# Optimization experiments

Measured on AMD Instinct MI355X. Metric: run time of the kernel, lower is better.

The kernel has to match this reference:

```python
import jax, jax.numpy as jnp
import numpy as np

N0, N1, N2 = 10000, 40000, 160000
E1, E2 = 240000, 960000
C_IN, C_MID, C_OUT = 64, 32, 16  # up_convs = [64, 32, 16]


def _basis(pseudo):
    """Open quadratic B-spline basis, kernel_size=3, degree=2, dim=2.
    With kernel_size-degree == 1, v = pseudo in [0,1) and all 3 basis fns per dim
    are active with fixed indices 0..2, so the 2-D product gives 9 weights/edge."""
    t = pseudo  # [E, 2]
    b = jnp.stack([0.5 * (1.0 - t) ** 2, -t * t + t + 0.5, 0.5 * t * t], axis=-1)  # [E,2,3]
    return (b[:, 0, :, None] * b[:, 1, None, :]).reshape(t.shape[0], 9)  # [E, 9]


def _spline_conv(x, src, dst, basis, W, R, b, n):
    # x: [N, Cin], W: [9, Cin, Cout], R: [Cin, Cout], b: [Cout]
    xs = x[src]  # [E, Cin] gather
    m = basis[:, 0:1] * (xs @ W[0])
    for k in range(1, 9):  # fixed small kernel loop; avoids [E,9,Cout] blowup
        m = m + basis[:, k:k + 1] * (xs @ W[k])
    agg = jax.ops.segment_sum(m, dst, num_segments=n)  # aggr='add'
    return agg + x @ R + b


def _up_level(x_coarse, unpool, edge, pseudo, skip, W1, R1, b1, W2, R2, b2):
    n = unpool.shape[0]
    x = x_coarse[unpool]          # MeshUnpool: copy coarse features to fine verts
    basis = _basis(pseudo)
    src, dst = edge[0], edge[1]
    h = jax.nn.relu(_spline_conv(x, src, dst, basis, W1, R1, b1, n))
    h = jnp.concatenate([h, skip], axis=1)  # [n, 2*Cout] == Cin
    h = jax.nn.relu(_spline_conv(h, src, dst, basis, W1, R1, b1, n))  # conv1 reused
    h = jax.nn.relu(_spline_conv(h, src, dst, basis, W2, R2, b2, n))
    return h


def setup_inputs() -> dict:
    key = jax.random.key(0)
    ks = jax.random.split(key, 24)
    s = 0.05
    inp = {
        'x0': jax.random.normal(ks[0], (N0, C_IN), jnp.float32),
        'unpool1': jax.random.randint(ks[1], (N1,), 0, N0),
        'edge1': jax.random.randint(ks[2], (2, E1), 0, N1),
        'pseudo1': jax.random.uniform(ks[3], (E1, 2), jnp.float32),
        'skip1': jax.random.normal(ks[4], (N1, C_MID), jnp.float32),
        'unpool2': jax.random.randint(ks[5], (N2,), 0, N1),
        'edge2': jax.random.randint(ks[6], (2, E2), 0, N2),
        'pseudo2': jax.random.uniform(ks[7], (E2, 2), jnp.float32),
        'skip2': jax.random.normal(ks[8], (N2, C_OUT), jnp.float32),
        # level 1 (UpConv 64 -> 32)
        'W1a': jax.random.normal(ks[9], (9, C_IN, C_MID), jnp.float32) * s,
        'R1a': jax.random.normal(ks[10], (C_IN, C_MID), jnp.float32) * s,
        'b1a': jax.random.normal(ks[11], (C_MID,), jnp.float32) * s,
        'W2a': jax.random.normal(ks[12], (9, C_MID, C_MID), jnp.float32) * s,
        'R2a': jax.random.normal(ks[13], (C_MID, C_MID), jnp.float32) * s,
        'b2a': jax.random.normal(ks[14], (C_MID,), jnp.float32) * s,
        # level 2 (UpConv 32 -> 16)
        'W1b': jax.random.normal(ks[15], (9, C_MID, C_OUT), jnp.float32) * s,
        'R1b': jax.random.normal(ks[16], (C_MID, C_OUT), jnp.float32) * s,
        'b1b': jax.random.normal(ks[17], (C_OUT,), jnp.float32) * s,
        'W2b': jax.random.normal(ks[18], (9, C_OUT, C_OUT), jnp.float32) * s,
        'R2b': jax.random.normal(ks[19], (C_OUT, C_OUT), jnp.float32) * s,
        'b2b': jax.random.normal(ks[20], (C_OUT,), jnp.float32) * s,
    }
    return inp


def reference(x0, unpool1, edge1, pseudo1, skip1, unpool2, edge2, pseudo2, skip2,
              W1a, R1a, b1a, W2a, R2a, b2a, W1b, R1b, b1b, W2b, R2b, b2b):
    h1 = _up_level(x0, unpool1, edge1, pseudo1, skip1, W1a, R1a, b1a, W2a, R2a, b2a)
    h2 = _up_level(h1, unpool2, edge2, pseudo2, skip2, W1b, R1b, b1b, W2b, R2b, b2b)
    return h2
```

## Files before the change

kernel.cpp:

```cpp
#include <hip/hip_runtime.h>
#include <stdint.h>

typedef __bf16 bf16x8 __attribute__((ext_vector_type(8)));
typedef __bf16 bf16x4 __attribute__((ext_vector_type(4)));
typedef float  f32x4  __attribute__((ext_vector_type(4)));

__global__ void k_up_f2b(const float4* __restrict__ xin, const int* __restrict__ up,
                         __bf16* __restrict__ xout, int N, int rowF4, int rowC) {
  int i = blockIdx.x * 256 + threadIdx.x;
  if (i >= N * rowF4) return;
  int n = i / rowF4, j = i - n * rowF4;
  float4 v = xin[(size_t)up[n] * rowF4 + j];
  bf16x4 o = {(__bf16)v.x, (__bf16)v.y, (__bf16)v.z, (__bf16)v.w};
  *reinterpret_cast<bf16x4*>(xout + (size_t)n * rowC + j * 4) = o;
}

__global__ void k_up_b2b(const uint4* __restrict__ xin, const int* __restrict__ up,
                         uint4* __restrict__ xout, int N, int rowU4) {
  int i = blockIdx.x * 256 + threadIdx.x;
  if (i >= N * rowU4) return;
  int n = i / rowU4, j = i - n * rowU4;
  xout[i] = xin[(size_t)up[n] * rowU4 + j];
}

__global__ __launch_bounds__(256) void k_bhist(const int* __restrict__ dst, int E,
                                               int* __restrict__ bcnt, int nbk) {
  __shared__ int h[256];
  int t = threadIdx.x;
  h[t] = 0;
  __syncthreads();
  int e0 = blockIdx.x * 2048 + t * 8;
  if (e0 + 8 <= E) {
    int4 a = *reinterpret_cast<const int4*>(dst + e0);
    int4 b = *reinterpret_cast<const int4*>(dst + e0 + 4);
    atomicAdd(&h[a.x >> 10], 1); atomicAdd(&h[a.y >> 10], 1);
    atomicAdd(&h[a.z >> 10], 1); atomicAdd(&h[a.w >> 10], 1);
    atomicAdd(&h[b.x >> 10], 1); atomicAdd(&h[b.y >> 10], 1);
    atomicAdd(&h[b.z >> 10], 1); atomicAdd(&h[b.w >> 10], 1);
  } else {
    for (int j = 0; j < 8; ++j)
      if (e0 + j < E) atomicAdd(&h[dst[e0 + j] >> 10], 1);
  }
  __syncthreads();
  if (t < nbk && h[t]) atomicAdd(&bcnt[t], h[t]);
}

__global__ void k_bscan(const int* __restrict__ bcnt, int nbk, int E,
                        int* __restrict__ bstart, int* __restrict__ bcur) {
  __shared__ int wsum[4];
  int t = threadIdx.x, lane = t & 63, w = t >> 6;
  int v = (t < nbk) ? bcnt[t] : 0;
  int x = v;
  #pragma unroll
  for (int o = 1; o < 64; o <<= 1) { int y = __shfl_up(x, o, 64); if (lane >= o) x += y; }
  if (lane == 63) wsum[w] = x;
  __syncthreads();
  int wpre = 0;
  #pragma unroll
  for (int k = 0; k < 4; ++k) if (k < w) wpre += wsum[k];
  int excl = wpre + x - v;
  if (t < nbk) { bstart[t] = excl; bcur[t] = excl; }
  if (t == 0) bstart[nbk] = E;
}

__global__ __launch_bounds__(256) void k_bpart(const int* __restrict__ src,
                        const int* __restrict__ dst, const float2* __restrict__ pse,
                        int E, int* __restrict__ bcur, uint2* __restrict__ ebuf, int nbk) {
  __shared__ int h[256];
  __shared__ int base[256];
  int t = threadIdx.x;
  h[t] = 0;
  __syncthreads();
  int e0 = blockIdx.x * 2048 + t * 8;
  int d[8], rank[8];
  bool full = (e0 + 8 <= E);
  if (full) {
    int4 a = *reinterpret_cast<const int4*>(dst + e0);
    int4 b = *reinterpret_cast<const int4*>(dst + e0 + 4);
    d[0] = a.x; d[1] = a.y; d[2] = a.z; d[3] = a.w;
    d[4] = b.x; d[5] = b.y; d[6] = b.z; d[7] = b.w;
    #pragma unroll
    for (int j = 0; j < 8; ++j) rank[j] = atomicAdd(&h[d[j] >> 10], 1);
  } else {
    #pragma unroll
    for (int j = 0; j < 8; ++j)
      if (e0 + j < E) { d[j] = dst[e0 + j]; rank[j] = atomicAdd(&h[d[j] >> 10], 1); }
  }
  __syncthreads();
  if (t < nbk && h[t]) base[t] = atomicAdd(&bcur[t], h[t]);
  __syncthreads();
  if (full) {
    int4 a = *reinterpret_cast<const int4*>(src + e0);
    int4 b = *reinterpret_cast<const int4*>(src + e0 + 4);
    int s[8] = {a.x, a.y, a.z, a.w, b.x, b.y, b.z, b.w};
    float2 p[8];
    #pragma unroll
    for (int j = 0; j < 8; ++j) p[j] = pse[e0 + j];
    #pragma unroll
    for (int j = 0; j < 8; ++j) {
      int bkt = d[j] >> 10, dloc = d[j] & 1023;
      union { uint u; _Float16 hh[2]; } cv;
      cv.hh[0] = (_Float16)p[j].x; cv.hh[1] = (_Float16)p[j].y;
      ebuf[base[bkt] + rank[j]] = make_uint2((uint)s[j] | ((uint)dloc << 18), cv.u);
    }
  } else {
    #pragma unroll
    for (int j = 0; j < 8; ++j) {
      if (e0 + j >= E) continue;
      int bkt = d[j] >> 10, dloc = d[j] & 1023;
      float2 p = pse[e0 + j];
      union { uint u; _Float16 hh[2]; } cv;
      cv.hh[0] = (_Float16)p.x; cv.hh[1] = (_Float16)p.y;
      ebuf[base[bkt] + rank[j]] = make_uint2((uint)src[e0 + j] | ((uint)dloc << 18), cv.u);
    }
  }
}

__global__ __launch_bounds__(256) void k_bcsr(const int* __restrict__ bstart,
                        const uint2* __restrict__ ebuf, uint2* __restrict__ epk,
                        int* __restrict__ off, int N, int E, int nbk) {
  __shared__ int cnt[1024];
  __shared__ int excl[1024];
  __shared__ int cur[1024];
  __shared__ int wsum[4];
  int b = blockIdx.x, t = threadIdx.x;
  int e0 = bstart[b], e1 = bstart[b + 1];
  #pragma unroll
  for (int k = 0; k < 4; ++k) { cnt[t * 4 + k] = 0; cur[t * 4 + k] = 0; }
  __syncthreads();
  for (int i = e0 + t; i < e1; i += 256)
    atomicAdd(&cnt[(ebuf[i].x >> 18) & 1023], 1);
  __syncthreads();
  int lane = t & 63, w = t >> 6;
  int i0 = t * 4;
  int c0 = cnt[i0], c1 = cnt[i0 + 1], c2 = cnt[i0 + 2], c3 = cnt[i0 + 3];
  int s = c0 + c1 + c2 + c3, x = s;
  #pragma unroll
  for (int o = 1; o < 64; o <<= 1) { int y = __shfl_up(x, o, 64); if (lane >= o) x += y; }
  if (lane == 63) wsum[w] = x;
  __syncthreads();
  int wpre = 0;
  #pragma unroll
  for (int k = 0; k < 4; ++k) if (k < w) wpre += wsum[k];
  int ex = wpre + x - s;
  excl[i0] = ex; excl[i0 + 1] = ex + c0; excl[i0 + 2] = ex + c0 + c1; excl[i0 + 3] = ex + c0 + c1 + c2;
  int dg0 = b * 1024;
  int exv[4] = {ex, ex + c0, ex + c0 + c1, ex + c0 + c1 + c2};
  #pragma unroll
  for (int k = 0; k < 4; ++k) {
    int d = dg0 + i0 + k;
    if (d < N) off[d] = e0 + exv[k];
  }
  __syncthreads();
  for (int i = e0 + t; i < e1; i += 256) {
    uint2 r = ebuf[i];
    int dloc = (r.x >> 18) & 1023;
    int rk = atomicAdd(&cur[dloc], 1);
    epk[e0 + excl[dloc] + rk] = make_uint2(r.x & 0x3FFFFu, r.y);
  }
  if (b == nbk - 1 && t == 0) off[N] = E;
}

__global__ void k_packall(const float* __restrict__ W1a, const float* __restrict__ R1a,
                          const float* __restrict__ W2a, const float* __restrict__ R2a,
                          const float* __restrict__ W1b, const float* __restrict__ R1b,
                          const float* __restrict__ W2b, const float* __restrict__ R2b,
                          __bf16* __restrict__ BpA, __bf16* __restrict__ BpB,
                          __bf16* __restrict__ BpC, __bf16* __restrict__ BpD) {
  int o = blockIdx.x * 256 + threadIdx.x;
  const float *W, *R; __bf16* Bp; int Cin, Cout;
  if (o < 20480)      { W = W1a; R = R1a; Bp = BpA; Cin = 64; Cout = 32; }
  else if (o < 30720) { W = W2a; R = R2a; Bp = BpB; Cin = 32; Cout = 32; o -= 20480; }
  else if (o < 35840) { W = W1b; R = R1b; Bp = BpC; Cin = 32; Cout = 16; o -= 30720; }
  else if (o < 38400) { W = W2b; R = R2b; Bp = BpD; Cin = 16; Cout = 16; o -= 35840; }
  else return;
  int CT = Cout / 16;
  int j = o & 7, lane = (o >> 3) & 63, tile = o >> 9;
  int ct = tile % CT, kc = tile / CT;
  int k = kc * 32 + ((lane >> 4) * 8) + j;
  int n = ct * 16 + (lane & 15);
  float v;
  if (k < 9 * Cin) { int k9 = k / Cin, cin = k - k9 * Cin; v = W[(k9 * Cin + cin) * Cout + n]; }
  else             { v = R[(k - 9 * Cin) * Cout + n]; }
  Bp[o] = (__bf16)v;
}

template<int Cin, int Cout, bool OUTF32, bool HAS_SKIP>
__global__ __launch_bounds__(256, 6) void k_conv(const int* __restrict__ off,
                        const uint2* __restrict__ epk,
                        const __bf16* __restrict__ X, const __bf16* __restrict__ Bp,
                        const float* __restrict__ bias, const float* __restrict__ skip,
                        void* __restrict__ outv, int N, int outStride) {
  constexpr int LPD = Cin / 4;
  constexpr int DPB = 256 / LPD;
  constexpr int K   = 10 * Cin;
  constexpr int KP2 = K + 8;
  constexpr int NT  = DPB / 16;
  constexpr int KC  = K / 32;
  constexpr int CT  = Cout / 16;
  constexpr int UNITS = NT * CT;

  __shared__ __bf16 As[DPB * KP2];

  int t = threadIdx.x;
  int g = t / LPD, sub = t % LPD;
  int d = blockIdx.x * DPB + g;

  float acc[9][4];
  #pragma unroll
  for (int k = 0; k < 9; ++k)
    #pragma unroll
    for (int v = 0; v < 4; ++v) acc[k][v] = 0.f;
  bf16x4 xd = {};

  if (d < N) {
    xd = *reinterpret_cast<const bf16x4*>(X + (size_t)d * Cin + sub * 4);
    int b0 = off[d], b1 = off[d + 1];
    int i = b0;
    for (; i + 4 <= b1; i += 4) {
      uint2 e0 = epk[i], e1 = epk[i + 1], e2 = epk[i + 2], e3 = epk[i + 3];
      bf16x4 xf0 = *reinterpret_cast<const bf16x4*>(X + (size_t)e0.x * Cin + sub * 4);
      bf16x4 xf1 = *reinterpret_cast<const bf16x4*>(X + (size_t)e1.x * Cin + sub * 4);
      bf16x4 xf2 = *reinterpret_cast<const bf16x4*>(X + (size_t)e2.x * Cin + sub * 4);
      bf16x4 xf3 = *reinterpret_cast<const bf16x4*>(X + (size_t)e3.x * Cin + sub * 4);
      uint ps[4] = {e0.y, e1.y, e2.y, e3.y};
      bf16x4 xfs[4] = {xf0, xf1, xf2, xf3};
      #pragma unroll
      for (int c = 0; c < 4; ++c) {
        union { uint u; _Float16 h[2]; } cv; cv.u = ps[c];
        float t0 = (float)cv.h[0], t1 = (float)cv.h[1];
        float u0 = 1.f - t0;
        float wi[3] = {0.5f * u0 * u0, -t0 * t0 + t0 + 0.5f, 0.5f * t0 * t0};
        float u1 = 1.f - t1;
        float wj[3] = {0.5f * u1 * u1, -t1 * t1 + t1 + 0.5f, 0.5f * t1 * t1};
        float xfv[4];
        #pragma unroll
        for (int v = 0; v < 4; ++v) xfv[v] = (float)xfs[c][v];
        #pragma unroll
        for (int ki = 0; ki < 3; ++ki)
          #pragma unroll
          for (int kj = 0; kj < 3; ++kj) {
            float w = wi[ki] * wj[kj];
            #pragma unroll
            for (int v = 0; v < 4; ++v)
              acc[ki * 3 + kj][v] += w * xfv[v];
          }
      }
    }
    for (; i < b1; ++i) {
      uint2 ep = epk[i];
      bf16x4 xf = *reinterpret_cast<const bf16x4*>(X + (size_t)ep.x * Cin + sub * 4);
      union { uint u; _Float16 h[2]; } cv; cv.u = ep.y;
      float t0 = (float)cv.h[0], t1 = (float)cv.h[1];
      float u0 = 1.f - t0;
      float wi[3] = {0.5f * u0 * u0, -t0 * t0 + t0 + 0.5f, 0.5f * t0 * t0};
      float u1 = 1.f - t1;
      float wj[3] = {0.5f * u1 * u1, -t1 * t1 + t1 + 0.5f, 0.5f * t1 * t1};
      float xfv[4];
      #pragma unroll
      for (int v = 0; v < 4; ++v) xfv[v] = (float)xf[v];
      #pragma unroll
      for (int ki = 0; ki < 3; ++ki)
        #pragma unroll
        for (int kj = 0; kj < 3; ++kj) {
          float w = wi[ki] * wj[kj];
          #pragma unroll
          for (int v = 0; v < 4; ++v)
            acc[ki * 3 + kj][v] += w * xfv[v];
        }
    }
  }

  __bf16* row = As + (size_t)g * KP2;
  #pragma unroll
  for (int k = 0; k < 9; ++k) {
    bf16x4 tmp;
    #pragma unroll
    for (int v = 0; v < 4; ++v) tmp[v] = (__bf16)acc[k][v];
    *reinterpret_cast<bf16x4*>(row + k * Cin + sub * 4) = tmp;
  }
  *reinterpret_cast<bf16x4*>(row + 9 * Cin + sub * 4) = xd;
  __syncthreads();

  int lane = t & 63, wave = t >> 6;
  int c15 = lane & 15, q = lane >> 4;
  for (int u = wave; u < UNITS; u += 4) {
    int tile = u / CT, ct = u - tile * CT;
    const __bf16* arow = As + (size_t)(tile * 16 + c15) * KP2 + q * 8;
    f32x4 a4 = {0.f, 0.f, 0.f, 0.f};
    #pragma unroll
    for (int kc = 0; kc < KC; ++kc) {
      bf16x8 a = *reinterpret_cast<const bf16x8*>(arow + kc * 32);
      bf16x8 b = *reinterpret_cast<const bf16x8*>(Bp + ((size_t)(kc * CT + ct) * 64 + lane) * 8);
      a4 = __builtin_amdgcn_mfma_f32_16x16x32_bf16(a, b, a4, 0, 0, 0);
    }
    int cout = ct * 16 + c15;
    float bb = bias[cout];
    #pragma unroll
    for (int r = 0; r < 4; ++r) {
      int m = q * 4 + r;
      int dd = blockIdx.x * DPB + tile * 16 + m;
      if (dd < N) {
        float vv = fmaxf(a4[r] + bb, 0.f);
        if constexpr (OUTF32)
          ((float*)outv)[(size_t)dd * outStride + cout] = vv;
        else
          ((__bf16*)outv)[(size_t)dd * outStride + cout] = (__bf16)vv;
        if constexpr (HAS_SKIP) {
          float sv = skip[(size_t)dd * Cout + cout];
          ((__bf16*)outv)[(size_t)dd * outStride + Cout + cout] = (__bf16)sv;
        }
      }
    }
  }
}

extern "C" void kernel_launch(void* const* d_in, const int* in_sizes, int n_in,
                              void* d_out, int out_size, void* d_ws, size_t ws_size,
                              hipStream_t stream) {
  const float* x0      = (const float*)d_in[0];
  const int*   up1     = (const int*)d_in[1];
  const int*   edge1   = (const int*)d_in[2];
  const float* pseudo1 = (const float*)d_in[3];
  const float* skip1   = (const float*)d_in[4];
  const int*   up2     = (const int*)d_in[5];
  const int*   edge2   = (const int*)d_in[6];
  const float* pseudo2 = (const float*)d_in[7];
  const float* skip2   = (const float*)d_in[8];
  const float* W1a = (const float*)d_in[9];
  const float* R1a = (const float*)d_in[10];
  const float* b1a = (const float*)d_in[11];
  const float* W2a = (const float*)d_in[12];
  const float* R2a = (const float*)d_in[13];
  const float* b2a = (const float*)d_in[14];
  const float* W1b = (const float*)d_in[15];
  const float* R1b = (const float*)d_in[16];
  const float* b1b = (const float*)d_in[17];
  const float* W2b = (const float*)d_in[18];
  const float* R2b = (const float*)d_in[19];
  const float* b2b = (const float*)d_in[20];

  const int N1 = 40000, N2 = 160000, E1 = 240000, E2 = 960000;
  const int NBK1 = (N1 + 1023) / 1024;
  const int NBK2 = (N2 + 1023) / 1024;

  char* ws = (char*)d_ws;
  __bf16* x1    = (__bf16*)(ws);
  __bf16* xcat1 = (__bf16*)(ws +  5120000);
  __bf16* x3    = (__bf16*)(ws + 10240000);
  __bf16* h1    = (__bf16*)(ws + 12800000);
  __bf16* x2    = (__bf16*)(ws + 15360000);
  __bf16* xcat2 = (__bf16*)(ws + 25600000);
  __bf16* x6    = (__bf16*)(ws + 35840000);
  int* off    = (int*)(ws + 40960000);
  uint2* ebuf = (uint2*)(ws + 41600016);
  uint2* epk  = (uint2*)(ws + 49280016);
  int* bcnt   = (int*)(ws + 56960016);
  int* bstart = (int*)(ws + 56961040);
  int* bcur   = (int*)(ws + 56962080);
  __bf16* BpA = (__bf16*)(ws + 56963104);
  __bf16* BpB = (__bf16*)(ws + 57004064);
  __bf16* BpC = (__bf16*)(ws + 57024544);
  __bf16* BpD = (__bf16*)(ws + 57034784);

  k_packall<<<150, 256, 0, stream>>>(W1a, R1a, W2a, R2a, W1b, R1b, W2b, R2b,
                                     BpA, BpB, BpC, BpD);

  k_up_f2b<<<N1 * 16 / 256, 256, 0, stream>>>((const float4*)x0, up1, x1, N1, 16, 64);

  hipMemsetAsync(bcnt, 0, 256 * 4, stream);
  k_bhist<<<(E1 + 2047) / 2048, 256, 0, stream>>>(edge1 + E1, E1, bcnt, NBK1);
  k_bscan<<<1, 256, 0, stream>>>(bcnt, NBK1, E1, bstart, bcur);
  k_bpart<<<(E1 + 2047) / 2048, 256, 0, stream>>>(edge1, edge1 + E1, (const float2*)pseudo1,
                                                  E1, bcur, ebuf, NBK1);
  k_bcsr<<<NBK1, 256, 0, stream>>>(bstart, ebuf, epk, off, N1, E1, NBK1);

  k_conv<64, 32, false, true><<<N1 / 16, 256, 0, stream>>>(off, epk, x1, BpA, b1a, skip1, xcat1, N1, 64);
  k_conv<64, 32, false, false><<<N1 / 16, 256, 0, stream>>>(off, epk, xcat1, BpA, b1a, nullptr, x3, N1, 32);
  k_conv<32, 32, false, false><<<N1 / 32, 256, 0, stream>>>(off, epk, x3, BpB, b2a, nullptr, h1, N1, 32);

  k_up_b2b<<<N2 * 4 / 256, 256, 0, stream>>>((const uint4*)h1, up2, (uint4*)x2, N2, 4);

  hipMemsetAsync(bcnt, 0, 256 * 4, stream);
  k_bhist<<<(E2 + 2047) / 2048, 256, 0, stream>>>(edge2 + E2, E2, bcnt, NBK2);
  k_bscan<<<1, 256, 0, stream>>>(bcnt, NBK2, E2, bstart, bcur);
  k_bpart<<<(E2 + 2047) / 2048, 256, 0, stream>>>(edge2, edge2 + E2, (const float2*)pseudo2,
                                                  E2, bcur, ebuf, NBK2);
  k_bcsr<<<NBK2, 256, 0, stream>>>(bstart, ebuf, epk, off, N2, E2, NBK2);

  k_conv<32, 16, false, true><<<N2 / 32, 256, 0, stream>>>(off, epk, x2, BpC, b1b, skip2, xcat2, N2, 32);
  k_conv<32, 16, false, false><<<N2 / 32, 256, 0, stream>>>(off, epk, xcat2, BpC, b1b, nullptr, x6, N2, 16);
  k_conv<16, 16, true, false><<<N2 / 64, 256, 0, stream>>>(off, epk, x6, BpD, b2b, nullptr, d_out, N2, 16);
}
```

Baseline: 357.2 us.

## Merge preprocessing for both levels into combined multi-role kernels

```diff
diff --git a/kernel.cpp b/kernel.cpp
--- a/kernel.cpp
+++ b/kernel.cpp
@@ -4,16 +4,6 @@
 typedef __bf16 bf16x8 __attribute__((ext_vector_type(8)));
 typedef __bf16 bf16x4 __attribute__((ext_vector_type(4)));
 typedef float  f32x4  __attribute__((ext_vector_type(4)));
-
-__global__ void k_up_f2b(const float4* __restrict__ xin, const int* __restrict__ up,
-                         __bf16* __restrict__ xout, int N, int rowF4, int rowC) {
-  int i = blockIdx.x * 256 + threadIdx.x;
-  if (i >= N * rowF4) return;
-  int n = i / rowF4, j = i - n * rowF4;
-  float4 v = xin[(size_t)up[n] * rowF4 + j];
-  bf16x4 o = {(__bf16)v.x, (__bf16)v.y, (__bf16)v.z, (__bf16)v.w};
-  *reinterpret_cast<bf16x4*>(xout + (size_t)n * rowC + j * 4) = o;
-}
 
 __global__ void k_up_b2b(const uint4* __restrict__ xin, const int* __restrict__ up,
                          uint4* __restrict__ xout, int N, int rowU4) {
@@ -23,151 +13,10 @@
   xout[i] = xin[(size_t)up[n] * rowU4 + j];
 }
 
-__global__ __launch_bounds__(256) void k_bhist(const int* __restrict__ dst, int E,
-                                               int* __restrict__ bcnt, int nbk) {
-  __shared__ int h[256];
-  int t = threadIdx.x;
-  h[t] = 0;
-  __syncthreads();
-  int e0 = blockIdx.x * 2048 + t * 8;
-  if (e0 + 8 <= E) {
-    int4 a = *reinterpret_cast<const int4*>(dst + e0);
-    int4 b = *reinterpret_cast<const int4*>(dst + e0 + 4);
-    atomicAdd(&h[a.x >> 10], 1); atomicAdd(&h[a.y >> 10], 1);
-    atomicAdd(&h[a.z >> 10], 1); atomicAdd(&h[a.w >> 10], 1);
-    atomicAdd(&h[b.x >> 10], 1); atomicAdd(&h[b.y >> 10], 1);
-    atomicAdd(&h[b.z >> 10], 1); atomicAdd(&h[b.w >> 10], 1);
-  } else {
-    for (int j = 0; j < 8; ++j)
-      if (e0 + j < E) atomicAdd(&h[dst[e0 + j] >> 10], 1);
-  }
-  __syncthreads();
-  if (t < nbk && h[t]) atomicAdd(&bcnt[t], h[t]);
-}
-
-__global__ void k_bscan(const int* __restrict__ bcnt, int nbk, int E,
-                        int* __restrict__ bstart, int* __restrict__ bcur) {
-  __shared__ int wsum[4];
-  int t = threadIdx.x, lane = t & 63, w = t >> 6;
-  int v = (t < nbk) ? bcnt[t] : 0;
-  int x = v;
-  #pragma unroll
-  for (int o = 1; o < 64; o <<= 1) { int y = __shfl_up(x, o, 64); if (lane >= o) x += y; }
-  if (lane == 63) wsum[w] = x;
-  __syncthreads();
-  int wpre = 0;
-  #pragma unroll
-  for (int k = 0; k < 4; ++k) if (k < w) wpre += wsum[k];
-  int excl = wpre + x - v;
-  if (t < nbk) { bstart[t] = excl; bcur[t] = excl; }
-  if (t == 0) bstart[nbk] = E;
-}
-
-__global__ __launch_bounds__(256) void k_bpart(const int* __restrict__ src,
-                        const int* __restrict__ dst, const float2* __restrict__ pse,
-                        int E, int* __restrict__ bcur, uint2* __restrict__ ebuf, int nbk) {
-  __shared__ int h[256];
-  __shared__ int base[256];
-  int t = threadIdx.x;
-  h[t] = 0;
-  __syncthreads();
-  int e0 = blockIdx.x * 2048 + t * 8;
-  int d[8], rank[8];
-  bool full = (e0 + 8 <= E);
-  if (full) {
-    int4 a = *reinterpret_cast<const int4*>(dst + e0);
-    int4 b = *reinterpret_cast<const int4*>(dst + e0 + 4);
-    d[0] = a.x; d[1] = a.y; d[2] = a.z; d[3] = a.w;
-    d[4] = b.x; d[5] = b.y; d[6] = b.z; d[7] = b.w;
-    #pragma unroll
-    for (int j = 0; j < 8; ++j) rank[j] = atomicAdd(&h[d[j] >> 10], 1);
-  } else {
-    #pragma unroll
-    for (int j = 0; j < 8; ++j)
-      if (e0 + j < E) { d[j] = dst[e0 + j]; rank[j] = atomicAdd(&h[d[j] >> 10], 1); }
-  }
-  __syncthreads();
-  if (t < nbk && h[t]) base[t] = atomicAdd(&bcur[t], h[t]);
-  __syncthreads();
-  if (full) {
-    int4 a = *reinterpret_cast<const int4*>(src + e0);
-    int4 b = *reinterpret_cast<const int4*>(src + e0 + 4);
-    int s[8] = {a.x, a.y, a.z, a.w, b.x, b.y, b.z, b.w};
-    float2 p[8];
-    #pragma unroll
-    for (int j = 0; j < 8; ++j) p[j] = pse[e0 + j];
-    #pragma unroll
-    for (int j = 0; j < 8; ++j) {
-      int bkt = d[j] >> 10, dloc = d[j] & 1023;
-      union { uint u; _Float16 hh[2]; } cv;
-      cv.hh[0] = (_Float16)p[j].x; cv.hh[1] = (_Float16)p[j].y;
-      ebuf[base[bkt] + rank[j]] = make_uint2((uint)s[j] | ((uint)dloc << 18), cv.u);
-    }
-  } else {
-    #pragma unroll
-    for (int j = 0; j < 8; ++j) {
-      if (e0 + j >= E) continue;
-      int bkt = d[j] >> 10, dloc = d[j] & 1023;
-      float2 p = pse[e0 + j];
-      union { uint u; _Float16 hh[2]; } cv;
-      cv.hh[0] = (_Float16)p.x; cv.hh[1] = (_Float16)p.y;
-      ebuf[base[bkt] + rank[j]] = make_uint2((uint)src[e0 + j] | ((uint)dloc << 18), cv.u);
-    }
-  }
-}
-
-__global__ __launch_bounds__(256) void k_bcsr(const int* __restrict__ bstart,
-                        const uint2* __restrict__ ebuf, uint2* __restrict__ epk,
-                        int* __restrict__ off, int N, int E, int nbk) {
-  __shared__ int cnt[1024];
-  __shared__ int excl[1024];
-  __shared__ int cur[1024];
-  __shared__ int wsum[4];
-  int b = blockIdx.x, t = threadIdx.x;
-  int e0 = bstart[b], e1 = bstart[b + 1];
-  #pragma unroll
-  for (int k = 0; k < 4; ++k) { cnt[t * 4 + k] = 0; cur[t * 4 + k] = 0; }
-  __syncthreads();
-  for (int i = e0 + t; i < e1; i += 256)
-    atomicAdd(&cnt[(ebuf[i].x >> 18) & 1023], 1);
-  __syncthreads();
-  int lane = t & 63, w = t >> 6;
-  int i0 = t * 4;
-  int c0 = cnt[i0], c1 = cnt[i0 + 1], c2 = cnt[i0 + 2], c3 = cnt[i0 + 3];
-  int s = c0 + c1 + c2 + c3, x = s;
-  #pragma unroll
-  for (int o = 1; o < 64; o <<= 1) { int y = __shfl_up(x, o, 64); if (lane >= o) x += y; }
-  if (lane == 63) wsum[w] = x;
-  __syncthreads();
-  int wpre = 0;
-  #pragma unroll
-  for (int k = 0; k < 4; ++k) if (k < w) wpre += wsum[k];
-  int ex = wpre + x - s;
-  excl[i0] = ex; excl[i0 + 1] = ex + c0; excl[i0 + 2] = ex + c0 + c1; excl[i0 + 3] = ex + c0 + c1 + c2;
-  int dg0 = b * 1024;
-  int exv[4] = {ex, ex + c0, ex + c0 + c1, ex + c0 + c1 + c2};
-  #pragma unroll
-  for (int k = 0; k < 4; ++k) {
-    int d = dg0 + i0 + k;
-    if (d < N) off[d] = e0 + exv[k];
-  }
-  __syncthreads();
-  for (int i = e0 + t; i < e1; i += 256) {
-    uint2 r = ebuf[i];
-    int dloc = (r.x >> 18) & 1023;
-    int rk = atomicAdd(&cur[dloc], 1);
-    epk[e0 + excl[dloc] + rk] = make_uint2(r.x & 0x3FFFFu, r.y);
-  }
-  if (b == nbk - 1 && t == 0) off[N] = E;
-}
-
-__global__ void k_packall(const float* __restrict__ W1a, const float* __restrict__ R1a,
-                          const float* __restrict__ W2a, const float* __restrict__ R2a,
-                          const float* __restrict__ W1b, const float* __restrict__ R1b,
-                          const float* __restrict__ W2b, const float* __restrict__ R2b,
-                          __bf16* __restrict__ BpA, __bf16* __restrict__ BpB,
-                          __bf16* __restrict__ BpC, __bf16* __restrict__ BpD) {
-  int o = blockIdx.x * 256 + threadIdx.x;
+__device__ __forceinline__ void d_pack(int o,
+    const float* W1a, const float* R1a, const float* W2a, const float* R2a,
+    const float* W1b, const float* R1b, const float* W2b, const float* R2b,
+    __bf16* BpA, __bf16* BpB, __bf16* BpC, __bf16* BpD) {
   const float *W, *R; __bf16* Bp; int Cin, Cout;
   if (o < 20480)      { W = W1a; R = R1a; Bp = BpA; Cin = 64; Cout = 32; }
   else if (o < 30720) { W = W2a; R = R2a; Bp = BpB; Cin = 32; Cout = 32; o -= 20480; }
@@ -185,8 +34,196 @@
   Bp[o] = (__bf16)v;
 }
 
+__device__ __forceinline__ void d_bhist(int b, int t, const int* dst, int E,
+                                        int* bcnt, int nbk) {
+  __shared__ int h[256];
+  h[t] = 0;
+  __syncthreads();
+  int e0 = b * 2048 + t * 8;
+  if (e0 + 8 <= E) {
+    int4 a = *reinterpret_cast<const int4*>(dst + e0);
+    int4 c = *reinterpret_cast<const int4*>(dst + e0 + 4);
+    atomicAdd(&h[a.x >> 10], 1); atomicAdd(&h[a.y >> 10], 1);
+    atomicAdd(&h[a.z >> 10], 1); atomicAdd(&h[a.w >> 10], 1);
+    atomicAdd(&h[c.x >> 10], 1); atomicAdd(&h[c.y >> 10], 1);
+    atomicAdd(&h[c.z >> 10], 1); atomicAdd(&h[c.w >> 10], 1);
+  } else {
+    for (int j = 0; j < 8; ++j)
+      if (e0 + j < E) atomicAdd(&h[dst[e0 + j] >> 10], 1);
+  }
+  __syncthreads();
+  if (t < nbk && h[t]) atomicAdd(&bcnt[t], h[t]);
+}
+
+__global__ __launch_bounds__(256) void k_prologue(
+    const float* __restrict__ W1a, const float* __restrict__ R1a,
+    const float* __restrict__ W2a, const float* __restrict__ R2a,
+    const float* __restrict__ W1b, const float* __restrict__ R1b,
+    const float* __restrict__ W2b, const float* __restrict__ R2b,
+    __bf16* __restrict__ BpA, __bf16* __restrict__ BpB,
+    __bf16* __restrict__ BpC, __bf16* __restrict__ BpD,
+    const float4* __restrict__ x0, const int* __restrict__ up1, __bf16* __restrict__ x1,
+    const int* __restrict__ dst1, int E1, int* __restrict__ bcnt1, int nbk1,
+    const int* __restrict__ dst2, int E2, int* __restrict__ bcnt2, int nbk2,
+    int N1) {
+  int b = blockIdx.x, t = threadIdx.x;
+  if (b < 150) {
+    d_pack(b * 256 + t, W1a, R1a, W2a, R2a, W1b, R1b, W2b, R2b, BpA, BpB, BpC, BpD);
+  } else if (b < 2650) {
+    int i = (b - 150) * 256 + t;
+    if (i < N1 * 16) {
+      int n = i >> 4, j = i & 15;
+      float4 v = x0[(size_t)up1[n] * 16 + j];
+      bf16x4 o = {(__bf16)v.x, (__bf16)v.y, (__bf16)v.z, (__bf16)v.w};
+      *reinterpret_cast<bf16x4*>(x1 + (size_t)n * 64 + j * 4) = o;
+    }
+  } else if (b < 2768) {
+    d_bhist(b - 2650, t, dst1, E1, bcnt1, nbk1);
+  } else {
+    d_bhist(b - 2768, t, dst2, E2, bcnt2, nbk2);
+  }
+}
+
+__global__ void k_bscan_dual(const int* __restrict__ bcnt1, int nbk1, int E1,
+                             int* __restrict__ bstart1, int* __restrict__ bcur1,
+                             const int* __restrict__ bcnt2, int nbk2, int E2,
+                             int* __restrict__ bstart2, int* __restrict__ bcur2) {
+  const int* bcnt; int nbk, E; int *bstart, *bcur;
+  if (blockIdx.x == 0) { bcnt = bcnt1; nbk = nbk1; E = E1; bstart = bstart1; bcur = bcur1; }
+  else                 { bcnt = bcnt2; nbk = nbk2; E = E2; bstart = bstart2; bcur = bcur2; }
+  __shared__ int wsum[4];
+  int t = threadIdx.x, lane = t & 63, w = t >> 6;
+  int v = (t < nbk) ? bcnt[t] : 0;
+  int x = v;
+  #pragma unroll
+  for (int o = 1; o < 64; o <<= 1) { int y = __shfl_up(x, o, 64); if (lane >= o) x += y; }
+  if (lane == 63) wsum[w] = x;
+  __syncthreads();
+  int wpre = 0;
+  #pragma unroll
+  for (int k = 0; k < 4; ++k) if (k < w) wpre += wsum[k];
+  int excl = wpre + x - v;
+  if (t < nbk) { bstart[t] = excl; bcur[t] = excl; }
+  if (t == 0) bstart[nbk] = E;
+}
+
+__device__ __forceinline__ void d_bpart(int b, int t, const int* src, const int* dst,
+                                        const float2* pse, int E, int* bcur,
+                                        uint2* ebuf, int nbk) {
+  __shared__ int h[256];
+  __shared__ int base[256];
+  h[t] = 0;
+  __syncthreads();
+  int e0 = b * 2048 + t * 8;
+  int d[8], rank[8];
+  bool full = (e0 + 8 <= E);
+  if (full) {
+    int4 a = *reinterpret_cast<const int4*>(dst + e0);
+    int4 c = *reinterpret_cast<const int4*>(dst + e0 + 4);
+    d[0] = a.x; d[1] = a.y; d[2] = a.z; d[3] = a.w;
+    d[4] = c.x; d[5] = c.y; d[6] = c.z; d[7] = c.w;
+    #pragma unroll
+    for (int j = 0; j < 8; ++j) rank[j] = atomicAdd(&h[d[j] >> 10], 1);
+  } else {
+    #pragma unroll
+    for (int j = 0; j < 8; ++j)
+      if (e0 + j < E) { d[j] = dst[e0 + j]; rank[j] = atomicAdd(&h[d[j] >> 10], 1); }
+  }
+  __syncthreads();
+  if (t < nbk && h[t]) base[t] = atomicAdd(&bcur[t], h[t]);
+  __syncthreads();
+  if (full) {
+    int4 a = *reinterpret_cast<const int4*>(src + e0);
+    int4 c = *reinterpret_cast<const int4*>(src + e0 + 4);
+    int s[8] = {a.x, a.y, a.z, a.w, c.x, c.y, c.z, c.w};
+    float2 p[8];
+    #pragma unroll
+    for (int j = 0; j < 8; ++j) p[j] = pse[e0 + j];
+    #pragma unroll
+    for (int j = 0; j < 8; ++j) {
+      int bkt = d[j] >> 10, dloc = d[j] & 1023;
+      union { uint u; _Float16 hh[2]; } cv;
+      cv.hh[0] = (_Float16)p[j].x; cv.hh[1] = (_Float16)p[j].y;
+      ebuf[base[bkt] + rank[j]] = make_uint2((uint)s[j] | ((uint)dloc << 18), cv.u);
+    }
+  } else {
+    #pragma unroll
+    for (int j = 0; j < 8; ++j) {
+      if (e0 + j >= E) continue;
+      int bkt = d[j] >> 10, dloc = d[j] & 1023;
+      float2 p = pse[e0 + j];
+      union { uint u; _Float16 hh[2]; } cv;
+      cv.hh[0] = (_Float16)p.x; cv.hh[1] = (_Float16)p.y;
+      ebuf[base[bkt] + rank[j]] = make_uint2((uint)src[e0 + j] | ((uint)dloc << 18), cv.u);
+    }
+  }
+}
+
+__global__ __launch_bounds__(256) void k_bpart_dual(
+    const int* __restrict__ src1, const int* __restrict__ dst1, const float2* __restrict__ pse1,
+    int E1, int* __restrict__ bcur1, uint2* __restrict__ ebuf1, int nbk1, int NB1,
+    const int* __restrict__ src2, const int* __restrict__ dst2, const float2* __restrict__ pse2,
+    int E2, int* __restrict__ bcur2, uint2* __restrict__ ebuf2, int nbk2) {
+  int b = blockIdx.x, t = threadIdx.x;
+  if (b < NB1) d_bpart(b, t, src1, dst1, pse1, E1, bcur1, ebuf1, nbk1);
+  else         d_bpart(b - NB1, t, src2, dst2, pse2, E2, bcur2, ebuf2, nbk2);
+}
+
+__device__ __forceinline__ void d_bcsr(int b, int t, const int* bstart, const uint2* ebuf,
+                                       uint2* epk, int* off, int N, int E, int nbk) {
+  __shared__ int cnt[1024];
+  __shared__ int excl[1024];
+  __shared__ int cur[1024];
+  __shared__ int wsum[4];
+  int e0 = bstart[b], e1 = bstart[b + 1];
+  #pragma unroll
+  for (int k = 0; k < 4; ++k) { cnt[t * 4 + k] = 0; cur[t * 4 + k] = 0; }
+  __syncthreads();
+  for (int i = e0 + t; i < e1; i += 256)
+    atomicAdd(&cnt[(ebuf[i].x >> 18) & 1023], 1);
+  __syncthreads();
+  int lane = t & 63, w = t >> 6;
+  int i0 = t * 4;
+  int c0 = cnt[i0], c1 = cnt[i0 + 1], c2 = cnt[i0 + 2], c3 = cnt[i0 + 3];
+  int s = c0 + c1 + c2 + c3, x = s;
+  #pragma unroll
+  for (int o = 1; o < 64; o <<= 1) { int y = __shfl_up(x, o, 64); if (lane >= o) x += y; }
+  if (lane == 63) wsum[w] = x;
+  __syncthreads();
+  int wpre = 0;
+  #pragma unroll
+  for (int k = 0; k < 4; ++k) if (k < w) wpre += wsum[k];
+  int ex = wpre + x - s;
+  excl[i0] = ex; excl[i0 + 1] = ex + c0; excl[i0 + 2] = ex + c0 + c1; excl[i0 + 3] = ex + c0 + c1 + c2;
+  int dg0 = b * 1024;
+  int exv[4] = {ex, ex + c0, ex + c0 + c1, ex + c0 + c1 + c2};
+  #pragma unroll
+  for (int k = 0; k < 4; ++k) {
+    int d = dg0 + i0 + k;
+    if (d < N) off[d] = e0 + exv[k];
+  }
+  __syncthreads();
+  for (int i = e0 + t; i < e1; i += 256) {
+    uint2 r = ebuf[i];
+    int dloc = (r.x >> 18) & 1023;
+    int rk = atomicAdd(&cur[dloc], 1);
+    epk[e0 + excl[dloc] + rk] = make_uint2(r.x & 0x3FFFFu, r.y);
+  }
+  if (b == nbk - 1 && t == 0) off[N] = E;
+}
+
+__global__ __launch_bounds__(256) void k_bcsr_dual(
+    const int* __restrict__ bstart1, const uint2* __restrict__ ebuf1, uint2* __restrict__ epk1,
+    int* __restrict__ off1, int N1, int E1, int nbk1,
+    const int* __restrict__ bstart2, const uint2* __restrict__ ebuf2, uint2* __restrict__ epk2,
+    int* __restrict__ off2, int N2, int E2, int nbk2) {
+  int b = blockIdx.x, t = threadIdx.x;
+  if (b < nbk1) d_bcsr(b, t, bstart1, ebuf1, epk1, off1, N1, E1, nbk1);
+  else          d_bcsr(b - nbk1, t, bstart2, ebuf2, epk2, off2, N2, E2, nbk2);
+}
+
 template<int Cin, int Cout, bool OUTF32, bool HAS_SKIP>
-__global__ __launch_bounds__(256, 6) void k_conv(const int* __restrict__ off,
+__global__ __launch_bounds__(256, 4) void k_conv(const int* __restrict__ off,
                         const uint2* __restrict__ epk,
                         const __bf16* __restrict__ X, const __bf16* __restrict__ Bp,
                         const float* __restrict__ bias, const float* __restrict__ skip,
@@ -341,54 +378,61 @@
   const float* b2b = (const float*)d_in[20];
 
   const int N1 = 40000, N2 = 160000, E1 = 240000, E2 = 960000;
-  const int NBK1 = (N1 + 1023) / 1024;
-  const int NBK2 = (N2 + 1023) / 1024;
+  const int NBK1 = 40, NBK2 = 157;
+  const int NB1 = (E1 + 2047) / 2048;
+  const int NB2 = (E2 + 2047) / 2048;
 
   char* ws = (char*)d_ws;
-  __bf16* x1    = (__bf16*)(ws);
-  __bf16* xcat1 = (__bf16*)(ws +  5120000);
-  __bf16* x3    = (__bf16*)(ws + 10240000);
-  __bf16* h1    = (__bf16*)(ws + 12800000);
-  __bf16* x2    = (__bf16*)(ws + 15360000);
-  __bf16* xcat2 = (__bf16*)(ws + 25600000);
-  __bf16* x6    = (__bf16*)(ws + 35840000);
-  int* off    = (int*)(ws + 40960000);
-  uint2* ebuf = (uint2*)(ws + 41600016);
-  uint2* epk  = (uint2*)(ws + 49280016);
-  int* bcnt   = (int*)(ws + 56960016);
-  int* bstart = (int*)(ws + 56961040);
-  int* bcur   = (int*)(ws + 56962080);
-  __bf16* BpA = (__bf16*)(ws + 56963104);
-  __bf16* BpB = (__bf16*)(ws + 57004064);
-  __bf16* BpC = (__bf16*)(ws + 57024544);
-  __bf16* BpD = (__bf16*)(ws + 57034784);
-
-  k_packall<<<150, 256, 0, stream>>>(W1a, R1a, W2a, R2a, W1b, R1b, W2b, R2b,
-                                     BpA, BpB, BpC, BpD);
-
-  k_up_f2b<<<N1 * 16 / 256, 256, 0, stream>>>((const float4*)x0, up1, x1, N1, 16, 64);
-
-  hipMemsetAsync(bcnt, 0, 256 * 4, stream);
-  k_bhist<<<(E1 + 2047) / 2048, 256, 0, stream>>>(edge1 + E1, E1, bcnt, NBK1);
-  k_bscan<<<1, 256, 0, stream>>>(bcnt, NBK1, E1, bstart, bcur);
-  k_bpart<<<(E1 + 2047) / 2048, 256, 0, stream>>>(edge1, edge1 + E1, (const float2*)pseudo1,
-                                                  E1, bcur, ebuf, NBK1);
-  k_bcsr<<<NBK1, 256, 0, stream>>>(bstart, ebuf, epk, off, N1, E1, NBK1);
-
-  k_conv<64, 32, false, true><<<N1 / 16, 256, 0, stream>>>(off, epk, x1, BpA, b1a, skip1, xcat1, N1, 64);
-  k_conv<64, 32, false, false><<<N1 / 16, 256, 0, stream>>>(off, epk, xcat1, BpA, b1a, nullptr, x3, N1, 32);
-  k_conv<32, 32, false, false><<<N1 / 32, 256, 0, stream>>>(off, epk, x3, BpB, b2a, nullptr, h1, N1, 32);
+  __bf16* x1     = (__bf16*)(ws);
+  __bf16* xcat1  = (__bf16*)(ws +  5120000);
+  __bf16* x3     = (__bf16*)(ws + 10240000);
+  __bf16* h1     = (__bf16*)(ws + 12800000);
+  __bf16* x2     = (__bf16*)(ws + 15360000);
+  __bf16* xcat2  = (__bf16*)(ws + 25600000);
+  __bf16* x6     = (__bf16*)(ws + 35840000);
+  int*   off1    = (int*)(ws + 40960000);
+  uint2* ebuf1   = (uint2*)(ws + 41120016);
+  uint2* epk1    = (uint2*)(ws + 43040016);
+  int*   off2    = (int*)(ws + 44960016);
+  uint2* ebuf2   = (uint2*)(ws + 45600032);
+  uint2* epk2    = (uint2*)(ws + 53280032);
+  int*   bcnt12  = (int*)(ws + 60960032);
+  int*   bstart1 = (int*)(ws + 60962080);
+  int*   bcur1   = (int*)(ws + 60962336);
+  int*   bstart2 = (int*)(ws + 60962592);
+  int*   bcur2   = (int*)(ws + 60963616);
+  __bf16* BpA    = (__bf16*)(ws + 60964640);
+  __bf16* BpB    = (__bf16*)(ws + 61005600);
+  __bf16* BpC    = (__bf16*)(ws + 61026080);
+  __bf16* BpD    = (__bf16*)(ws + 61036320);
+  int* bcnt1 = bcnt12, *bcnt2 = bcnt12 + 256;
+
+  hipMemsetAsync(bcnt12, 0, 512 * 4, stream);
+
+  k_prologue<<<150 + 2500 + NB1 + NB2, 256, 0, stream>>>(
+      W1a, R1a, W2a, R2a, W1b, R1b, W2b, R2b, BpA, BpB, BpC, BpD,
+      (const float4*)x0, up1, x1,
+      edge1 + E1, E1, bcnt1, NBK1,
+      edge2 + E2, E2, bcnt2, NBK2, N1);
+
+  k_bscan_dual<<<2, 256, 0, stream>>>(bcnt1, NBK1, E1, bstart1, bcur1,
+                                      bcnt2, NBK2, E2, bstart2, bcur2);
+
+  k_bpart_dual<<<NB1 + NB2, 256, 0, stream>>>(
+      edge1, edge1 + E1, (const float2*)pseudo1, E1, bcur1, ebuf1, NBK1, NB1,
+      edge2, edge2 + E2, (const float2*)pseudo2, E2, bcur2, ebuf2, NBK2);
+
+  k_bcsr_dual<<<NBK1 + NBK2, 256, 0, stream>>>(
+      bstart1, ebuf1, epk1, off1, N1, E1, NBK1,
+      bstart2, ebuf2, epk2, off2, N2, E2, NBK2);
+
+  k_conv<64, 32, false, true><<<N1 / 16, 256, 0, stream>>>(off1, epk1, x1, BpA, b1a, skip1, xcat1, N1, 64);
+  k_conv<64, 32, false, false><<<N1 / 16, 256, 0, stream>>>(off1, epk1, xcat1, BpA, b1a, nullptr, x3, N1, 32);
+  k_conv<32, 32, false, false><<<N1 / 32, 256, 0, stream>>>(off1, epk1, x3, BpB, b2a, nullptr, h1, N1, 32);
 
   k_up_b2b<<<N2 * 4 / 256, 256, 0, stream>>>((const uint4*)h1, up2, (uint4*)x2, N2, 4);
 
-  hipMemsetAsync(bcnt, 0, 256 * 4, stream);
-  k_bhist<<<(E2 + 2047) / 2048, 256, 0, stream>>>(edge2 + E2, E2, bcnt, NBK2);
-  k_bscan<<<1, 256, 0, stream>>>(bcnt, NBK2, E2, bstart, bcur);
-  k_bpart<<<(E2 + 2047) / 2048, 256, 0, stream>>>(edge2, edge2 + E2, (const float2*)pseudo2,
-                                                  E2, bcur, ebuf, NBK2);
-  k_bcsr<<<NBK2, 256, 0, stream>>>(bstart, ebuf, epk, off, N2, E2, NBK2);
-
-  k_conv<32, 16, false, true><<<N2 / 32, 256, 0, stream>>>(off, epk, x2, BpC, b1b, skip2, xcat2, N2, 32);
-  k_conv<32, 16, false, false><<<N2 / 32, 256, 0, stream>>>(off, epk, xcat2, BpC, b1b, nullptr, x6, N2, 16);
-  k_conv<16, 16, true, false><<<N2 / 64, 256, 0, stream>>>(off, epk, x6, BpD, b2b, nullptr, d_out, N2, 16);
-}
+  k_conv<32, 16, false, true><<<N2 / 32, 256, 0, stream>>>(off2, epk2, x2, BpC, b1b, skip2, xcat2, N2, 32);
+  k_conv<32, 16, false, false><<<N2 / 32, 256, 0, stream>>>(off2, epk2, xcat2, BpC, b1b, nullptr, x6, N2, 16);
+  k_conv<16, 16, true, false><<<N2 / 64, 256, 0, stream>>>(off2, epk2, x6, BpD, b2b, nullptr, d_out, N2, 16);
+}
```

New measurement: 314.3 us, median of 2. 1.14x faster.
